# Performance work log

Measured on AMD Instinct MI355X. Metric: run time of the kernel, lower is better.

## Reference

```python
import jax, jax.numpy as jnp
import numpy as np

B = 1024      # number of states
NP = 32       # SVGD particles per state
AD = 20       # act_dim
OD = 64       # obs_dim
H = 256       # critic hidden width
STEPS = 5     # num_svgd_steps
LR = 0.1      # svgd_lr (adaptive_lr disabled)
SP0 = 1.0     # svgd_sigma_p0
ALIM = 1.0    # act_limit


def _q(obs, X, w1, b1, w2, b2, w3, b3):
    h = jnp.concatenate([obs, X], axis=-1)
    h = jax.nn.relu(h @ w1 + b1)
    h = jax.nn.relu(h @ w2 + b2)
    return jnp.squeeze(h @ w3 + b3, -1)


def _rbf(X):
    # X: [B, NP, AD] -> K [B,NP,NP], diff [B,NP,NP,AD], gamma [B,1,1], K_grad [B,NP,NP,AD]
    diff = X[:, :, None, :] - X[:, None, :, :]
    dist_sq = jnp.sum(diff * diff, axis=-1)
    # adaptive bandwidth via median heuristic (adaptive_sig=True)
    med = jnp.median(dist_sq.reshape(dist_sq.shape[0], -1), axis=-1)
    sig_sq = med / (2.0 * jnp.log(NP + 1.0))
    gamma = (1.0 / (2.0 * sig_sq + 1e-8))[:, None, None]
    K = jnp.exp(-gamma * dist_sq)
    K_grad = -2.0 * gamma[..., None] * diff * K[..., None]  # d/dx_i K(x_i, x_j)
    return K, diff, gamma, K_grad


def setup_inputs():
    key = jax.random.key(0)
    ks = jax.random.split(key, 16)
    N = B * NP

    def lin(k, fi, fo):
        return (jax.random.normal(k, (fi, fo), jnp.float32) / np.sqrt(fi)).astype(jnp.float32)

    return {
        "obs": jax.random.normal(ks[0], (N, OD), jnp.float32),
        "a0": jax.random.normal(ks[1], (N, AD), jnp.float32) * np.sqrt(SP0),
        "q1_w1": lin(ks[2], OD + AD, H), "q1_b1": jnp.zeros((H,), jnp.float32),
        "q1_w2": lin(ks[3], H, H),       "q1_b2": jnp.zeros((H,), jnp.float32),
        "q1_w3": lin(ks[4], H, 1),       "q1_b3": jnp.zeros((1,), jnp.float32),
        "q2_w1": lin(ks[5], OD + AD, H), "q2_b1": jnp.zeros((H,), jnp.float32),
        "q2_w2": lin(ks[6], H, H),       "q2_b2": jnp.zeros((H,), jnp.float32),
        "q2_w3": lin(ks[7], H, 1),       "q2_b3": jnp.zeros((1,), jnp.float32),
    }


def reference(obs, a0, q1_w1, q1_b1, q1_w2, q1_b2, q1_w3, q1_b3,
              q2_w1, q2_b1, q2_w2, q2_b2, q2_w3, q2_b3):
    eye = jnp.eye(NP, dtype=a0.dtype)

    def q_min_sum(Xf):
        q1 = _q(obs, Xf, q1_w1, q1_b1, q1_w2, q1_b2, q1_w3, q1_b3)
        q2 = _q(obs, Xf, q2_w1, q2_b1, q2_w2, q2_b2, q2_w3, q2_b3)
        return jnp.sum(jnp.minimum(q1, q2))

    score_fn = jax.grad(q_min_sum)  # autograd score function

    def step(carry, _):
        a, logp = carry
        score = score_fn(a).reshape(-1, NP, AD)                 # [B,NP,AD]
        X = a.reshape(-1, NP, AD)
        K, diff, gamma, Kg = _rbf(X)
        phi = (jnp.einsum('bij,bjd->bid', K, score) + Kg.sum(axis=1)) / NP
        # log-prob correction terms (with_logprob=True)
        term1 = jnp.mean(jnp.sum(Kg * score[:, None, :, :], axis=-1), axis=2)     # [B,NP]
        inner = jnp.sum(jnp.transpose(Kg, (0, 2, 1, 3)) * diff, axis=-1) \
                - AD * (K - eye)
        term2 = -2.0 * gamma[:, :, 0] * jnp.mean(inner, axis=1)                   # [B,NP]
        logp = logp - LR * (term1 + term2)
        a = a + LR * phi.reshape(a.shape)                        # svgd_optim
        return (a, logp), None

    logp0 = jnp.zeros((B, NP), a0.dtype)
    (a, logp_svgd), _ = jax.lax.scan(step, (a0, logp0), None, length=STEPS)

    a_sq = ALIM * jnp.tanh(a)                                    # [B*NP, AD]
    logp_normal = (-AD * 0.5 * jnp.log(2.0 * jnp.pi * SP0)
                   - 0.5 / SP0 * jnp.sum(a0 * a0, axis=-1)).reshape(-1, NP)
    logp_tanh = -jnp.sum(2.0 * (jnp.log(2.0) - a - jax.nn.softplus(-2.0 * a)),
                         axis=-1).reshape(-1, NP)
    logp_a = jnp.mean(logp_normal + logp_svgd + logp_tanh, axis=-1)  # [B]
    return a_sq, logp_a
```

## Files before the change

kernel.cpp:

```cpp
#include <hip/hip_runtime.h>
#include <math.h>

#define NPART 32
#define ADIM  20
#define ODIM  64
#define HID   256
#define NSTEPS 5
#define LRC   0.1f
#define NBLK  512
#define LOG33 3.4965075614664802f
#define A0LD  104

typedef short bf8 __attribute__((ext_vector_type(8)));
typedef short s4b __attribute__((ext_vector_type(4)));
typedef float f4  __attribute__((ext_vector_type(4)));
typedef unsigned u4 __attribute__((ext_vector_type(4)));

#define OW1T(n) ((n)*24576)
#define OW2T(n) (49152 + (n)*65536)
#define OW2C(n) (180224 + (n)*65536)
#define OW1X(n) (311296 + (n)*8192)
#define WS_ELEMS 327680

__device__ __forceinline__ short f2bf(float x) {
    unsigned u = __float_as_uint(x);
    u += 0x7FFFu + ((u >> 16) & 1u);
    return (short)(u >> 16);
}
__device__ __forceinline__ short f2bfT(float x) {
    return (short)(__float_as_uint(x) >> 16);
}
__device__ __forceinline__ float bf2f(short s) {
    return __uint_as_float(((unsigned)(unsigned short)s) << 16);
}

#define MFMA(a,b,c) __builtin_amdgcn_mfma_f32_16x16x32_bf16((a),(b),(c),0,0,0)

__global__ void prep_weights(const float* __restrict__ w1a, const float* __restrict__ w2a,
                             const float* __restrict__ w3a, const float* __restrict__ w1b,
                             const float* __restrict__ w2b, const float* __restrict__ w3b,
                             unsigned short* __restrict__ ws)
{
    int idx = blockIdx.x * 256 + threadIdx.x;
    if (idx >= WS_ELEMS) return;
    float val;
    if (idx < 49152) {
        int net = idx / 24576, rem = idx % 24576;
        int n = rem / 96, k = rem % 96;
        const float* w1 = net ? w1b : w1a;
        val = (k < 84) ? w1[k*256 + n] : 0.f;
    } else if (idx < 180224) {
        int t2 = idx - 49152; int net = t2 / 65536, rem = t2 % 65536;
        int n = rem / 256, k = rem % 256;
        const float* w2 = net ? w2b : w2a;
        val = w2[k*256 + n];
    } else if (idx < 311296) {
        int t2 = idx - 180224; int net = t2 / 65536, rem = t2 % 65536;
        const float* w2 = net ? w2b : w2a;
        const float* w3 = net ? w3b : w3a;
        val = w2[rem] * w3[rem % 256];
    } else {
        int t2 = idx - 311296; int net = t2 / 8192, rem = t2 % 8192;
        int d = rem / 256, n = rem % 256;
        const float* w1 = net ? w1b : w1a;
        val = (d < 20) ? w1[(64 + d)*256 + n] : 0.f;
    }
    ws[idx] = (unsigned short)f2bf(val);
}

__global__ void __launch_bounds__(512, 4)
svgd_main(const float* __restrict__ obs,  const float* __restrict__ a0g,
          const float* __restrict__ b1a,  const float* __restrict__ b2a, const float* __restrict__ b3a,
          const float* __restrict__ b1b,  const float* __restrict__ b2b, const float* __restrict__ b3b,
          const float* __restrict__ w3af, const float* __restrict__ w3bf,
          const unsigned short* __restrict__ ws, float* __restrict__ out)
{
    __shared__ __align__(16) short A0s[64*A0LD];
    __shared__ __align__(16) short hbuf[64*264];
    __shared__ unsigned maskS[2][2][64][8];
    __shared__ float Xm[64*20];
    __shared__ float scoreS[64*21];
    __shared__ float qpart[2][8][64];
    __shared__ int   winsS[64];
    __shared__ float logps[64];
    __shared__ unsigned short lutI[496], lutJ[496];
    __shared__ float med2[4];
    __shared__ float qvS[64];
    __shared__ float normsS[64], rowKS[64];
    __shared__ __align__(16) float diagS[64];

    float* d2sF = (float*)hbuf;
    float* GSF  = ((float*)hbuf) + 2304;
    short* SBs  = hbuf + 9216;
    short* KbS  = hbuf + 9216;
    short* STbS = hbuf + 11776;
    short* XTbS = hbuf + 14336;

    const int t = threadIdx.x, b = blockIdx.x;
    const int lane = t & 63, wv = t >> 6;
    const int q = lane >> 4, mp = lane & 15;
    const int nb = wv * 32;

    for (int p = t; p < 64*ODIM; p += 512) {
        int i = p >> 6, d = p & 63;
        A0s[i*A0LD + d] = f2bfT(obs[(b*64 + i)*ODIM + d]);
    }
    for (int p = t; p < 64*ADIM; p += 512) {
        int i = p / 20, d = p - i*20;
        float v = a0g[(b*64 + i)*20 + d];
        Xm[p] = v;
        A0s[i*A0LD + 64 + d] = f2bfT(v);
    }
    for (int p = t; p < 64*12; p += 512) { int i = p/12, d = p - i*12; A0s[i*A0LD + 84 + d] = 0; }
    if (t < 496) {
        int i_ = 0, rem = t;
        while (rem >= 31 - i_) { rem -= 31 - i_; ++i_; }
        lutI[t] = (unsigned short)i_; lutJ[t] = (unsigned short)(i_ + 1 + rem);
    }
    if (t < 64) logps[t] = 0.f;
    __syncthreads();

    for (int step = 0; step < NSTEPS; ++step) {
        for (int net = 0; net < 2; ++net) {
            const unsigned short* w1t = ws + OW1T(net);
            const unsigned short* w2t = ws + OW2T(net);
            const float* b1p = net ? b1b : b1a;
            const float* b2p = net ? b2b : b2a;
            const float* w3p = net ? w3bf : w3af;

            f4 acc[4][2];
            #pragma unroll
            for (int h = 0; h < 4; ++h) { acc[h][0] = (f4){0,0,0,0}; acc[h][1] = (f4){0,0,0,0}; }
            {
                const unsigned short* bp0 = w1t + (size_t)(nb +      mp)*96 + q*8;
                const unsigned short* bp1 = w1t + (size_t)(nb + 16 + mp)*96 + q*8;
                bf8 bb0 = *(const bf8*)bp0, bb1 = *(const bf8*)bp1;
                #pragma unroll
                for (int k0 = 0; k0 < 96; k0 += 32) {
                    bf8 n0 = bb0, n1 = bb1;
                    if (k0 + 32 < 96) { n0 = *(const bf8*)(bp0 + k0 + 32); n1 = *(const bf8*)(bp1 + k0 + 32); }
                    #pragma unroll
                    for (int h = 0; h < 4; ++h) {
                        bf8 aa = *(const bf8*)&A0s[(h*16 + mp)*A0LD + k0 + q*8];
                        acc[h][0] = MFMA(aa, bb0, acc[h][0]);
                        acc[h][1] = MFMA(aa, bb1, acc[h][1]);
                    }
                    bb0 = n0; bb1 = n1;
                }
            }
            {
                float bias0 = b1p[nb + mp], bias1 = b1p[nb + 16 + mp];
                #pragma unroll
                for (int h = 0; h < 4; ++h) {
                    #pragma unroll
                    for (int r = 0; r < 4; ++r) {
                        float v0 = acc[h][0][r] + bias0;
                        float v1 = acc[h][1][r] + bias1;
                        bool p0 = v0 > 0.f, p1 = v1 > 0.f;
                        unsigned long long bal0 = __ballot(p0);
                        unsigned long long bal1 = __ballot(p1);
                        int row = h*16 + q*4 + r;
                        hbuf[row*264 + nb +      mp] = f2bfT(p0 ? v0 : 0.f);
                        hbuf[row*264 + nb + 16 + mp] = f2bfT(p1 ? v1 : 0.f);
                        if (mp == 0) {
                            unsigned w = (unsigned)((bal0 >> (q*16)) & 0xFFFFull)
                                       | (((unsigned)((bal1 >> (q*16)) & 0xFFFFull)) << 16);
                            maskS[net][0][row][wv] = w;
                        }
                    }
                }
            }
            __syncthreads();

            #pragma unroll
            for (int h = 0; h < 4; ++h) { acc[h][0] = (f4){0,0,0,0}; acc[h][1] = (f4){0,0,0,0}; }
            {
                const unsigned short* bp0 = w2t + (size_t)(nb +      mp)*256 + q*8;
                const unsigned short* bp1 = w2t + (size_t)(nb + 16 + mp)*256 + q*8;
                bf8 bb0 = *(const bf8*)bp0, bb1 = *(const bf8*)bp1;
                #pragma unroll
                for (int k0 = 0; k0 < 256; k0 += 32) {
                    bf8 n0 = bb0, n1 = bb1;
                    if (k0 + 32 < 256) { n0 = *(const bf8*)(bp0 + k0 + 32); n1 = *(const bf8*)(bp1 + k0 + 32); }
                    #pragma unroll
                    for (int h = 0; h < 4; ++h) {
                        bf8 aa = *(const bf8*)&hbuf[(h*16 + mp)*264 + k0 + q*8];
                        acc[h][0] = MFMA(aa, bb0, acc[h][0]);
                        acc[h][1] = MFMA(aa, bb1, acc[h][1]);
                    }
                    bb0 = n0; bb1 = n1;
                }
            }
            {
                float bias0 = b2p[nb + mp], bias1 = b2p[nb + 16 + mp];
                float w30   = w3p[nb + mp], w31   = w3p[nb + 16 + mp];
                float qp[4][4] = {{0,0,0,0},{0,0,0,0},{0,0,0,0},{0,0,0,0}};
                #pragma unroll
                for (int h = 0; h < 4; ++h) {
                    #pragma unroll
                    for (int r = 0; r < 4; ++r) {
                        float v0 = acc[h][0][r] + bias0;
                        float v1 = acc[h][1][r] + bias1;
                        bool p0 = v0 > 0.f, p1 = v1 > 0.f;
                        unsigned long long bal0 = __ballot(p0);
                        unsigned long long bal1 = __ballot(p1);
                        if (mp == 0) {
                            unsigned w = (unsigned)((bal0 >> (q*16)) & 0xFFFFull)
                                       | (((unsigned)((bal1 >> (q*16)) & 0xFFFFull)) << 16);
                            maskS[net][1][h*16 + q*4 + r][wv] = w;
                        }
                        qp[h][r] += (p0 ? v0 * w30 : 0.f) + (p1 ? v1 * w31 : 0.f);
                    }
                }
                #pragma unroll
                for (int d = 1; d < 16; d <<= 1)
                    #pragma unroll
                    for (int h = 0; h < 4; ++h)
                        #pragma unroll
                        for (int r = 0; r < 4; ++r)
                            qp[h][r] += __shfl_xor(qp[h][r], d, 64);
                if (mp == 0) {
                    #pragma unroll
                    for (int h = 0; h < 4; ++h)
                        #pragma unroll
                        for (int r = 0; r < 4; ++r)
                            qpart[net][wv][h*16 + q*4 + r] = qp[h][r];
                }
            }
            __syncthreads();
        }

        if (t < 64) {
            float q0 = b3a[0], q1 = b3b[0];
            #pragma unroll
            for (int w = 0; w < 8; ++w) { q0 += qpart[0][w][t]; q1 += qpart[1][w][t]; }
            winsS[t] = (q0 <= q1) ? 0 : 1;
        }
        __syncthreads();

        for (int net = 0; net < 2; ++net) {
            const unsigned short* w2c = ws + OW2C(net);

            f4 acc[4][2];
            #pragma unroll
            for (int h = 0; h < 4; ++h) { acc[h][0] = (f4){0,0,0,0}; acc[h][1] = (f4){0,0,0,0}; }
            int win[4];
            #pragma unroll
            for (int h = 0; h < 4; ++h) win[h] = (winsS[h*16 + mp] == net);
            {
                const unsigned short* bp0 = w2c + (size_t)(nb +      mp)*256 + q*8;
                const unsigned short* bp1 = w2c + (size_t)(nb + 16 + mp)*256 + q*8;
                bf8 bb0 = *(const bf8*)bp0, bb1 = *(const bf8*)bp1;
                #pragma unroll
                for (int k0 = 0; k0 < 256; k0 += 32) {
                    bf8 n0 = bb0, n1 = bb1;
                    if (k0 + 32 < 256) { n0 = *(const bf8*)(bp0 + k0 + 32); n1 = *(const bf8*)(bp1 + k0 + 32); }
                    #pragma unroll
                    for (int h = 0; h < 4; ++h) {
                        unsigned bits = win[h] ? ((maskS[net][1][h*16 + mp][k0 >> 5] >> (q*8)) & 0xFFu) : 0u;
                        u4 mw;
                        mw[0] = ((bits &   1u) ? 0x3F80u : 0u) | ((bits &   2u) ? 0x3F800000u : 0u);
                        mw[1] = ((bits &   4u) ? 0x3F80u : 0u) | ((bits &   8u) ? 0x3F800000u : 0u);
                        mw[2] = ((bits &  16u) ? 0x3F80u : 0u) | ((bits &  32u) ? 0x3F800000u : 0u);
                        mw[3] = ((bits &  64u) ? 0x3F80u : 0u) | ((bits & 128u) ? 0x3F800000u : 0u);
                        bf8 aa = __builtin_bit_cast(bf8, mw);
                        acc[h][0] = MFMA(aa, bb0, acc[h][0]);
                        acc[h][1] = MFMA(aa, bb1, acc[h][1]);
                    }
                    bb0 = n0; bb1 = n1;
                }
            }
            #pragma unroll
            for (int h = 0; h < 4; ++h) {
                #pragma unroll
                for (int s = 0; s < 2; ++s) {
                    int col = nb + s*16 + mp;
                    #pragma unroll
                    for (int r = 0; r < 4; ++r) {
                        int row = h*16 + q*4 + r;
                        bool on = (maskS[net][0][row][col >> 5] >> (col & 31)) & 1u;
                        hbuf[row*264 + col] = f2bfT(on ? acc[h][s][r] : 0.f);
                    }
                }
            }
            __syncthreads();
            {
                int mt = wv & 3, ch = wv >> 2;
                const unsigned short* w1x = ws + OW1X(net);
                const unsigned short* bp  = w1x + (size_t)(ch*16 + mp)*256 + q*8;
                f4 sa = (f4){0,0,0,0};
                bf8 bx = *(const bf8*)bp;
                #pragma unroll
                for (int k0 = 0; k0 < 256; k0 += 32) {
                    bf8 nx = bx;
                    if (k0 + 32 < 256) nx = *(const bf8*)(bp + k0 + 32);
                    bf8 aa = *(const bf8*)&hbuf[(mt*16 + mp)*264 + k0 + q*8];
                    sa = MFMA(aa, bx, sa);
                    bx = nx;
                }
                int colD = ch*16 + mp;
                if (colD < 20) {
                    #pragma unroll
                    for (int r = 0; r < 4; ++r) {
                        int row = mt*16 + q*4 + r;
                        if (net == 0) scoreS[row*21 + colD]  = sa[r];
                        else          scoreS[row*21 + colD] += sa[r];
                    }
                }
            }
            __syncthreads();
        }

        if (t < 64) {
            int st = t >> 5;
            float nrm = 0.f, dg = 0.f;
            #pragma unroll
            for (int d = 0; d < 20; ++d) {
                float xb = bf2f(A0s[t*A0LD + 64 + d]);
                nrm += xb * xb;
                float sv = scoreS[t*21 + d];
                float xv = Xm[t*20 + d];
                dg += xv * sv;
                short sb = f2bfT(sv);
                SBs[t*40 + d] = sb;
                STbS[st*1280 + d*40 + (t & 31)] = sb;
                XTbS[st*1280 + d*40 + (t & 31)] = f2bfT(xv);
            }
            #pragma unroll
            for (int d = 20; d < 32; ++d) SBs[t*40 + d] = 0;
            normsS[t] = nrm;
            diagS[t]  = dg;
        }
        __syncthreads();

        {
            int stw = wv >> 2, mt = (wv >> 1) & 1, nt = wv & 1;
            bf8 aa  = *(const bf8*)&A0s[(stw*32 + mt*16 + mp)*A0LD + 64 + q*8];
            bf8 bbx = *(const bf8*)&A0s[(stw*32 + nt*16 + mp)*A0LD + 64 + q*8];
            bf8 bbs = *(const bf8*)&SBs[(stw*32 + nt*16 + mp)*40 + q*8];
            f4 gx = MFMA(aa, bbx, ((f4){0,0,0,0}));
            f4 gs = MFMA(aa, bbs, ((f4){0,0,0,0}));
            int jl = nt*16 + mp;
            float nj = normsS[stw*32 + jl];
            #pragma unroll
            for (int r = 0; r < 4; ++r) {
                int il = mt*16 + q*4 + r;
                d2sF[stw*1152 + il*36 + jl] = normsS[stw*32 + il] + nj - 2.f*gx[r];
                GSF [stw*1152 + il*36 + jl] = gs[r];
            }
        }
        __syncthreads();

        if (wv < 2) {
            const float* base = d2sF + wv*1152;
            float v[8];
            #pragma unroll
            for (int i = 0; i < 8; ++i) {
                int e = lane*8 + i;
                v[i] = (e < 496) ? base[lutI[e]*36 + lutJ[e]] : 3.4e38f;
            }
            for (int k = 2; k <= 512; k <<= 1) {
                for (int jj = k >> 1; jj >= 8; jj >>= 1) {
                    int lm = jj >> 3;
                    #pragma unroll
                    for (int i = 0; i < 8; ++i) {
                        float w = __shfl_xor(v[i], lm, 64);
                        int p = lane*8 + i;
                        bool takeMin = (((p & k) == 0) == ((p & jj) == 0));
                        v[i] = takeMin ? fminf(v[i], w) : fmaxf(v[i], w);
                    }
                }
                int jj0 = (k >> 1) < 4 ? (k >> 1) : 4;
                for (int jj = jj0; jj >= 1; jj >>= 1) {
                    #pragma unroll
                    for (int i = 0; i < 8; ++i) {
                        if ((i & jj) == 0) {
                            int i2 = i | jj;
                            int p = lane*8 + i;
                            bool up = ((p & k) == 0);
                            float x = v[i], y = v[i2];
                            float mn = fminf(x, y), mx = fmaxf(x, y);
                            v[i] = up ? mn : mx; v[i2] = up ? mx : mn;
                        }
                    }
                }
            }
            if (lane == 29) med2[wv*2 + 0] = v[7];
            if (lane == 30) med2[wv*2 + 1] = v[0];
        }
        __syncthreads();

        {
            int i = t >> 3, stw = i >> 5, il = i & 31, j0 = (t & 7) * 4;
            float medv = 0.5f * (med2[stw*2] + med2[stw*2 + 1]);
            float gam  = 1.f / (2.f * (medv / (2.f * LOG33)) + 1e-8f);
            f4 d2 = *(const f4*)&d2sF[stw*1152 + il*36 + j0];
            f4 gs = *(const f4*)&GSF [stw*1152 + il*36 + j0];
            f4 dg = *(const f4*)&diagS[stw*32 + j0];
            float K0 = expf(-gam * d2[0]), K1 = expf(-gam * d2[1]);
            float K2 = expf(-gam * d2[2]), K3 = expf(-gam * d2[3]);
            s4b kb; kb[0] = f2bfT(K0); kb[1] = f2bfT(K1); kb[2] = f2bfT(K2); kb[3] = f2bfT(K3);
            *(s4b*)&KbS[stw*1280 + il*40 + j0] = kb;
            float sK   = K0 + K1 + K2 + K3;
            float sKGS = K0*gs[0] + K1*gs[1] + K2*gs[2] + K3*gs[3];
            float sKd2 = K0*d2[0] + K1*d2[1] + K2*d2[2] + K3*d2[3];
            float sKdg = K0*dg[0] + K1*dg[1] + K2*dg[2] + K3*dg[3];
            #pragma unroll
            for (int d = 1; d < 8; d <<= 1) {
                sK   += __shfl_xor(sK,   d, 64);
                sKGS += __shfl_xor(sKGS, d, 64);
                sKd2 += __shfl_xor(sKd2, d, 64);
                sKdg += __shfl_xor(sKdg, d, 64);
            }
            if ((t & 7) == 0) {
                rowKS[i] = sK;
                float sdots = sKGS - sKdg;
                float ssum  = -2.f*gam*sdots
                              - 2.f*gam*(2.f*gam*sKd2 - 20.f*(sK - 1.f));
                logps[i] -= LRC * (ssum * (1.f/32.f));
            }
        }
        __syncthreads();

        {
            int stw = wv >> 2, mt = (wv >> 1) & 1, nt = wv & 1;
            float medv = 0.5f * (med2[stw*2] + med2[stw*2 + 1]);
            float gam  = 1.f / (2.f * (medv / (2.f * LOG33)) + 1e-8f);
            bf8 aa  = *(const bf8*)&KbS [stw*1280 + (mt*16 + mp)*40 + q*8];
            bf8 b1v = *(const bf8*)&STbS[stw*1280 + (nt*16 + mp)*40 + q*8];
            bf8 b2v = *(const bf8*)&XTbS[stw*1280 + (nt*16 + mp)*40 + q*8];
            f4 ks = MFMA(aa, b1v, ((f4){0,0,0,0}));
            f4 kx = MFMA(aa, b2v, ((f4){0,0,0,0}));
            int dd = nt*16 + mp;
            if (dd < 20) {
                #pragma unroll
                for (int r = 0; r < 4; ++r) {
                    int gi = stw*32 + mt*16 + q*4 + r;
                    float xi  = Xm[gi*20 + dd];
                    float phi = (ks[r] + 2.f*gam*(xi*rowKS[gi] - kx[r])) * (1.f/32.f);
                    float nx  = xi + LRC * phi;
                    Xm[gi*20 + dd] = nx;
                    A0s[gi*A0LD + 64 + dd] = f2bfT(nx);
                }
            }
        }
        __syncthreads();
    }

    for (int p = t; p < 64*20; p += 512) {
        int i = p / 20, d = p - i*20;
        out[(b*64 + i)*20 + d] = tanhf(Xm[p]);
    }
    if (t < 64) {
        float lt = 0.f, s0 = 0.f;
        for (int d = 0; d < 20; ++d) {
            float a  = Xm[t*20 + d];
            float x  = -2.f * a;
            float sp = fmaxf(x, 0.f) + log1pf(expf(-fabsf(x)));
            lt -= 2.f * (0.69314718056f - a - sp);
            float v = a0g[(b*64 + t)*20 + d];
            s0 += v * v;
        }
        qvS[t] = -18.3787706641f - 0.5f*s0 + logps[t] + lt;
    }
    __syncthreads();
    if (t < 2) {
        float s = 0.f;
        for (int i = 0; i < 32; ++i) s += qvS[t*32 + i];
        out[1024*32*20 + b*2 + t] = s * (1.f/32.f);
    }
}

extern "C" void kernel_launch(void* const* d_in, const int* in_sizes, int n_in,
                              void* d_out, int out_size, void* d_ws, size_t ws_size,
                              hipStream_t stream) {
    unsigned short* ws = (unsigned short*)d_ws;
    prep_weights<<<(WS_ELEMS + 255)/256, 256, 0, stream>>>(
        (const float*)d_in[2],  (const float*)d_in[4],  (const float*)d_in[6],
        (const float*)d_in[8],  (const float*)d_in[10], (const float*)d_in[12], ws);
    svgd_main<<<NBLK, 512, 0, stream>>>(
        (const float*)d_in[0],  (const float*)d_in[1],
        (const float*)d_in[3],  (const float*)d_in[5],  (const float*)d_in[7],
        (const float*)d_in[9],  (const float*)d_in[11], (const float*)d_in[13],
        (const float*)d_in[6],  (const float*)d_in[12],
        ws, (float*)d_out);
}
```

Measured before the change: 488.5 us.

## Process one state per block with 256 threads and wider per-wave N tiles

```diff
diff --git a/kernel.cpp b/kernel.cpp
--- a/kernel.cpp
+++ b/kernel.cpp
@@ -1,13 +1,9 @@
 #include <hip/hip_runtime.h>
 #include <math.h>
 
-#define NPART 32
-#define ADIM  20
-#define ODIM  64
-#define HID   256
 #define NSTEPS 5
 #define LRC   0.1f
-#define NBLK  512
+#define NBLK  1024
 #define LOG33 3.4965075614664802f
 #define A0LD  104
 
@@ -68,56 +64,55 @@
     ws[idx] = (unsigned short)f2bf(val);
 }
 
-__global__ void __launch_bounds__(512, 4)
+__global__ void __launch_bounds__(256, 4)
 svgd_main(const float* __restrict__ obs,  const float* __restrict__ a0g,
           const float* __restrict__ b1a,  const float* __restrict__ b2a, const float* __restrict__ b3a,
           const float* __restrict__ b1b,  const float* __restrict__ b2b, const float* __restrict__ b3b,
           const float* __restrict__ w3af, const float* __restrict__ w3bf,
           const unsigned short* __restrict__ ws, float* __restrict__ out)
 {
-    __shared__ __align__(16) short A0s[64*A0LD];
-    __shared__ __align__(16) short hbuf[64*264];
-    __shared__ unsigned maskS[2][2][64][8];
-    __shared__ float Xm[64*20];
-    __shared__ float scoreS[64*21];
-    __shared__ float qpart[2][8][64];
-    __shared__ int   winsS[64];
-    __shared__ float logps[64];
+    __shared__ __align__(16) short A0s[32*A0LD];
+    __shared__ __align__(16) short hbuf[32*264];
+    __shared__ unsigned maskS[2][2][32][9];
+    __shared__ float Xm[32*20];
+    __shared__ float scoreS[32*21];
+    __shared__ float qpart[2][4][32];
+    __shared__ float logps[32];
     __shared__ unsigned short lutI[496], lutJ[496];
-    __shared__ float med2[4];
-    __shared__ float qvS[64];
-    __shared__ float normsS[64], rowKS[64];
-    __shared__ __align__(16) float diagS[64];
+    __shared__ float med2[2];
+    __shared__ float qvS[32];
+    __shared__ float normsS[32], rowKS[32];
+    __shared__ __align__(16) float diagS[32];
 
     float* d2sF = (float*)hbuf;
-    float* GSF  = ((float*)hbuf) + 2304;
-    short* SBs  = hbuf + 9216;
-    short* KbS  = hbuf + 9216;
-    short* STbS = hbuf + 11776;
-    short* XTbS = hbuf + 14336;
+    float* GSF  = ((float*)hbuf) + 1152;
+    short* SBs  = hbuf + 4608;
+    short* KbS  = hbuf + 4608;
+    short* STbS = hbuf + 5888;
+    short* XTbS = hbuf + 7168;
 
     const int t = threadIdx.x, b = blockIdx.x;
     const int lane = t & 63, wv = t >> 6;
     const int q = lane >> 4, mp = lane & 15;
-    const int nb = wv * 32;
-
-    for (int p = t; p < 64*ODIM; p += 512) {
+    const int nb = wv * 64;
+
+    for (int p = t; p < 32*64; p += 256) {
         int i = p >> 6, d = p & 63;
-        A0s[i*A0LD + d] = f2bfT(obs[(b*64 + i)*ODIM + d]);
-    }
-    for (int p = t; p < 64*ADIM; p += 512) {
+        A0s[i*A0LD + d] = f2bfT(obs[(b*32 + i)*64 + d]);
+    }
+    for (int p = t; p < 32*20; p += 256) {
         int i = p / 20, d = p - i*20;
-        float v = a0g[(b*64 + i)*20 + d];
+        float v = a0g[(b*32 + i)*20 + d];
         Xm[p] = v;
         A0s[i*A0LD + 64 + d] = f2bfT(v);
     }
-    for (int p = t; p < 64*12; p += 512) { int i = p/12, d = p - i*12; A0s[i*A0LD + 84 + d] = 0; }
-    if (t < 496) {
-        int i_ = 0, rem = t;
+    for (int p = t; p < 32*12; p += 256) { int i = p/12, d = p - i*12; A0s[i*A0LD + 84 + d] = 0; }
+    for (int p = t; p < 496; p += 256) {
+        int i_ = 0, rem = p;
         while (rem >= 31 - i_) { rem -= 31 - i_; ++i_; }
-        lutI[t] = (unsigned short)i_; lutJ[t] = (unsigned short)(i_ + 1 + rem);
-    }
-    if (t < 64) logps[t] = 0.f;
+        lutI[p] = (unsigned short)i_; lutJ[p] = (unsigned short)(i_ + 1 + rem);
+    }
+    if (t < 32) logps[t] = 0.f;
     __syncthreads();
 
     for (int step = 0; step < NSTEPS; ++step) {
@@ -128,100 +123,110 @@
             const float* b2p = net ? b2b : b2a;
             const float* w3p = net ? w3bf : w3af;
 
-            f4 acc[4][2];
-            #pragma unroll
-            for (int h = 0; h < 4; ++h) { acc[h][0] = (f4){0,0,0,0}; acc[h][1] = (f4){0,0,0,0}; }
             {
-                const unsigned short* bp0 = w1t + (size_t)(nb +      mp)*96 + q*8;
-                const unsigned short* bp1 = w1t + (size_t)(nb + 16 + mp)*96 + q*8;
-                bf8 bb0 = *(const bf8*)bp0, bb1 = *(const bf8*)bp1;
+                f4 acc[2][4];
+                #pragma unroll
+                for (int h = 0; h < 2; ++h)
+                    #pragma unroll
+                    for (int s = 0; s < 4; ++s) acc[h][s] = (f4){0,0,0,0};
                 #pragma unroll
                 for (int k0 = 0; k0 < 96; k0 += 32) {
-                    bf8 n0 = bb0, n1 = bb1;
-                    if (k0 + 32 < 96) { n0 = *(const bf8*)(bp0 + k0 + 32); n1 = *(const bf8*)(bp1 + k0 + 32); }
-                    #pragma unroll
-                    for (int h = 0; h < 4; ++h) {
+                    bf8 bb[4];
+                    #pragma unroll
+                    for (int s = 0; s < 4; ++s)
+                        bb[s] = *(const bf8*)(w1t + (size_t)(nb + s*16 + mp)*96 + k0 + q*8);
+                    #pragma unroll
+                    for (int h = 0; h < 2; ++h) {
                         bf8 aa = *(const bf8*)&A0s[(h*16 + mp)*A0LD + k0 + q*8];
-                        acc[h][0] = MFMA(aa, bb0, acc[h][0]);
-                        acc[h][1] = MFMA(aa, bb1, acc[h][1]);
-                    }
-                    bb0 = n0; bb1 = n1;
-                }
-            }
+                        #pragma unroll
+                        for (int s = 0; s < 4; ++s) acc[h][s] = MFMA(aa, bb[s], acc[h][s]);
+                    }
+                }
+                float bias[4];
+                #pragma unroll
+                for (int s = 0; s < 4; ++s) bias[s] = b1p[nb + s*16 + mp];
+                #pragma unroll
+                for (int h = 0; h < 2; ++h) {
+                    #pragma unroll
+                    for (int r = 0; r < 4; ++r) {
+                        unsigned long long bal[4];
+                        #pragma unroll
+                        for (int s = 0; s < 4; ++s) {
+                            float v = acc[h][s][r] + bias[s];
+                            bool pos = v > 0.f;
+                            bal[s] = __ballot(pos);
+                            hbuf[(h*16 + q*4 + r)*264 + nb + s*16 + mp] = f2bfT(pos ? v : 0.f);
+                        }
+                        if (mp == 0) {
+                            int row = h*16 + q*4 + r;
+                            unsigned w01 = (unsigned)((bal[0] >> (q*16)) & 0xFFFFull)
+                                         | (((unsigned)((bal[1] >> (q*16)) & 0xFFFFull)) << 16);
+                            unsigned w23 = (unsigned)((bal[2] >> (q*16)) & 0xFFFFull)
+                                         | (((unsigned)((bal[3] >> (q*16)) & 0xFFFFull)) << 16);
+                            maskS[net][0][row][wv*2 + 0] = w01;
+                            maskS[net][0][row][wv*2 + 1] = w23;
+                        }
+                    }
+                }
+            }
+            __syncthreads();
+
             {
-                float bias0 = b1p[nb + mp], bias1 = b1p[nb + 16 + mp];
-                #pragma unroll
-                for (int h = 0; h < 4; ++h) {
+                f4 acc[2][4];
+                #pragma unroll
+                for (int h = 0; h < 2; ++h)
+                    #pragma unroll
+                    for (int s = 0; s < 4; ++s) acc[h][s] = (f4){0,0,0,0};
+                #pragma unroll
+                for (int k0 = 0; k0 < 256; k0 += 32) {
+                    bf8 bb[4];
+                    #pragma unroll
+                    for (int s = 0; s < 4; ++s)
+                        bb[s] = *(const bf8*)(w2t + (size_t)(nb + s*16 + mp)*256 + k0 + q*8);
+                    #pragma unroll
+                    for (int h = 0; h < 2; ++h) {
+                        bf8 aa = *(const bf8*)&hbuf[(h*16 + mp)*264 + k0 + q*8];
+                        #pragma unroll
+                        for (int s = 0; s < 4; ++s) acc[h][s] = MFMA(aa, bb[s], acc[h][s]);
+                    }
+                }
+                float bias[4], w3v[4];
+                #pragma unroll
+                for (int s = 0; s < 4; ++s) { bias[s] = b2p[nb + s*16 + mp]; w3v[s] = w3p[nb + s*16 + mp]; }
+                float qp[2][4] = {{0,0,0,0},{0,0,0,0}};
+                #pragma unroll
+                for (int h = 0; h < 2; ++h) {
                     #pragma unroll
                     for (int r = 0; r < 4; ++r) {
-                        float v0 = acc[h][0][r] + bias0;
-                        float v1 = acc[h][1][r] + bias1;
-                        bool p0 = v0 > 0.f, p1 = v1 > 0.f;
-                        unsigned long long bal0 = __ballot(p0);
-                        unsigned long long bal1 = __ballot(p1);
-                        int row = h*16 + q*4 + r;
-                        hbuf[row*264 + nb +      mp] = f2bfT(p0 ? v0 : 0.f);
-                        hbuf[row*264 + nb + 16 + mp] = f2bfT(p1 ? v1 : 0.f);
+                        unsigned long long bal[4];
+                        #pragma unroll
+                        for (int s = 0; s < 4; ++s) {
+                            float v = acc[h][s][r] + bias[s];
+                            bool pos = v > 0.f;
+                            bal[s] = __ballot(pos);
+                            qp[h][r] += pos ? v * w3v[s] : 0.f;
+                        }
                         if (mp == 0) {
-                            unsigned w = (unsigned)((bal0 >> (q*16)) & 0xFFFFull)
-                                       | (((unsigned)((bal1 >> (q*16)) & 0xFFFFull)) << 16);
-                            maskS[net][0][row][wv] = w;
+                            int row = h*16 + q*4 + r;
+                            unsigned w01 = (unsigned)((bal[0] >> (q*16)) & 0xFFFFull)
+                                         | (((unsigned)((bal[1] >> (q*16)) & 0xFFFFull)) << 16);
+                            unsigned w23 = (unsigned)((bal[2] >> (q*16)) & 0xFFFFull)
+                                         | (((unsigned)((bal[3] >> (q*16)) & 0xFFFFull)) << 16);
+                            maskS[net][1][row][wv*2 + 0] = w01;
+                            maskS[net][1][row][wv*2 + 1] = w23;
                         }
                     }
                 }
-            }
-            __syncthreads();
-
-            #pragma unroll
-            for (int h = 0; h < 4; ++h) { acc[h][0] = (f4){0,0,0,0}; acc[h][1] = (f4){0,0,0,0}; }
-            {
-                const unsigned short* bp0 = w2t + (size_t)(nb +      mp)*256 + q*8;
-                const unsigned short* bp1 = w2t + (size_t)(nb + 16 + mp)*256 + q*8;
-                bf8 bb0 = *(const bf8*)bp0, bb1 = *(const bf8*)bp1;
-                #pragma unroll
-                for (int k0 = 0; k0 < 256; k0 += 32) {
-                    bf8 n0 = bb0, n1 = bb1;
-                    if (k0 + 32 < 256) { n0 = *(const bf8*)(bp0 + k0 + 32); n1 = *(const bf8*)(bp1 + k0 + 32); }
-                    #pragma unroll
-                    for (int h = 0; h < 4; ++h) {
-                        bf8 aa = *(const bf8*)&hbuf[(h*16 + mp)*264 + k0 + q*8];
-                        acc[h][0] = MFMA(aa, bb0, acc[h][0]);
-                        acc[h][1] = MFMA(aa, bb1, acc[h][1]);
-                    }
-                    bb0 = n0; bb1 = n1;
-                }
-            }
-            {
-                float bias0 = b2p[nb + mp], bias1 = b2p[nb + 16 + mp];
-                float w30   = w3p[nb + mp], w31   = w3p[nb + 16 + mp];
-                float qp[4][4] = {{0,0,0,0},{0,0,0,0},{0,0,0,0},{0,0,0,0}};
-                #pragma unroll
-                for (int h = 0; h < 4; ++h) {
-                    #pragma unroll
-                    for (int r = 0; r < 4; ++r) {
-                        float v0 = acc[h][0][r] + bias0;
-                        float v1 = acc[h][1][r] + bias1;
-                        bool p0 = v0 > 0.f, p1 = v1 > 0.f;
-                        unsigned long long bal0 = __ballot(p0);
-                        unsigned long long bal1 = __ballot(p1);
-                        if (mp == 0) {
-                            unsigned w = (unsigned)((bal0 >> (q*16)) & 0xFFFFull)
-                                       | (((unsigned)((bal1 >> (q*16)) & 0xFFFFull)) << 16);
-                            maskS[net][1][h*16 + q*4 + r][wv] = w;
-                        }
-                        qp[h][r] += (p0 ? v0 * w30 : 0.f) + (p1 ? v1 * w31 : 0.f);
-                    }
-                }
                 #pragma unroll
                 for (int d = 1; d < 16; d <<= 1)
                     #pragma unroll
-                    for (int h = 0; h < 4; ++h)
+                    for (int h = 0; h < 2; ++h)
                         #pragma unroll
                         for (int r = 0; r < 4; ++r)
                             qp[h][r] += __shfl_xor(qp[h][r], d, 64);
                 if (mp == 0) {
                     #pragma unroll
-                    for (int h = 0; h < 4; ++h)
+                    for (int h = 0; h < 2; ++h)
                         #pragma unroll
                         for (int r = 0; r < 4; ++r)
                             qpart[net][wv][h*16 + q*4 + r] = qp[h][r];
@@ -230,73 +235,71 @@
             __syncthreads();
         }
 
-        if (t < 64) {
-            float q0 = b3a[0], q1 = b3b[0];
+        int winf[2][2];
+        {
+            float ba = b3a[0], bb_ = b3b[0];
             #pragma unroll
-            for (int w = 0; w < 8; ++w) { q0 += qpart[0][w][t]; q1 += qpart[1][w][t]; }
-            winsS[t] = (q0 <= q1) ? 0 : 1;
-        }
-        __syncthreads();
-
+            for (int h = 0; h < 2; ++h) {
+                int row = h*16 + mp;
+                float q0 = ba, q1 = bb_;
+                #pragma unroll
+                for (int w = 0; w < 4; ++w) { q0 += qpart[0][w][row]; q1 += qpart[1][w][row]; }
+                winf[0][h] = (q0 <= q1) ? 1 : 0;
+                winf[1][h] = 1 - winf[0][h];
+            }
+        }
+        #pragma unroll
         for (int net = 0; net < 2; ++net) {
             const unsigned short* w2c = ws + OW2C(net);
-
-            f4 acc[4][2];
-            #pragma unroll
-            for (int h = 0; h < 4; ++h) { acc[h][0] = (f4){0,0,0,0}; acc[h][1] = (f4){0,0,0,0}; }
-            int win[4];
-            #pragma unroll
-            for (int h = 0; h < 4; ++h) win[h] = (winsS[h*16 + mp] == net);
             {
-                const unsigned short* bp0 = w2c + (size_t)(nb +      mp)*256 + q*8;
-                const unsigned short* bp1 = w2c + (size_t)(nb + 16 + mp)*256 + q*8;
-                bf8 bb0 = *(const bf8*)bp0, bb1 = *(const bf8*)bp1;
+                f4 acc[2][4];
+                #pragma unroll
+                for (int h = 0; h < 2; ++h)
+                    #pragma unroll
+                    for (int s = 0; s < 4; ++s) acc[h][s] = (f4){0,0,0,0};
                 #pragma unroll
                 for (int k0 = 0; k0 < 256; k0 += 32) {
-                    bf8 n0 = bb0, n1 = bb1;
-                    if (k0 + 32 < 256) { n0 = *(const bf8*)(bp0 + k0 + 32); n1 = *(const bf8*)(bp1 + k0 + 32); }
-                    #pragma unroll
-                    for (int h = 0; h < 4; ++h) {
-                        unsigned bits = win[h] ? ((maskS[net][1][h*16 + mp][k0 >> 5] >> (q*8)) & 0xFFu) : 0u;
+                    bf8 bb[4];
+                    #pragma unroll
+                    for (int s = 0; s < 4; ++s)
+                        bb[s] = *(const bf8*)(w2c + (size_t)(nb + s*16 + mp)*256 + k0 + q*8);
+                    #pragma unroll
+                    for (int h = 0; h < 2; ++h) {
+                        unsigned bits = winf[net][h] ? ((maskS[net][1][h*16 + mp][k0 >> 5] >> (q*8)) & 0xFFu) : 0u;
                         u4 mw;
                         mw[0] = ((bits &   1u) ? 0x3F80u : 0u) | ((bits &   2u) ? 0x3F800000u : 0u);
                         mw[1] = ((bits &   4u) ? 0x3F80u : 0u) | ((bits &   8u) ? 0x3F800000u : 0u);
                         mw[2] = ((bits &  16u) ? 0x3F80u : 0u) | ((bits &  32u) ? 0x3F800000u : 0u);
                         mw[3] = ((bits &  64u) ? 0x3F80u : 0u) | ((bits & 128u) ? 0x3F800000u : 0u);
                         bf8 aa = __builtin_bit_cast(bf8, mw);
-                        acc[h][0] = MFMA(aa, bb0, acc[h][0]);
-                        acc[h][1] = MFMA(aa, bb1, acc[h][1]);
-                    }
-                    bb0 = n0; bb1 = n1;
-                }
-            }
-            #pragma unroll
-            for (int h = 0; h < 4; ++h) {
-                #pragma unroll
-                for (int s = 0; s < 2; ++s) {
-                    int col = nb + s*16 + mp;
-                    #pragma unroll
-                    for (int r = 0; r < 4; ++r) {
-                        int row = h*16 + q*4 + r;
-                        bool on = (maskS[net][0][row][col >> 5] >> (col & 31)) & 1u;
-                        hbuf[row*264 + col] = f2bfT(on ? acc[h][s][r] : 0.f);
+                        #pragma unroll
+                        for (int s = 0; s < 4; ++s) acc[h][s] = MFMA(aa, bb[s], acc[h][s]);
+                    }
+                }
+                #pragma unroll
+                for (int h = 0; h < 2; ++h) {
+                    #pragma unroll
+                    for (int s = 0; s < 4; ++s) {
+                        int col = nb + s*16 + mp;
+                        #pragma unroll
+                        for (int r = 0; r < 4; ++r) {
+                            int row = h*16 + q*4 + r;
+                            bool on = (maskS[net][0][row][col >> 5] >> (col & 31)) & 1u;
+                            hbuf[row*264 + col] = f2bfT(on ? acc[h][s][r] : 0.f);
+                        }
                     }
                 }
             }
             __syncthreads();
             {
-                int mt = wv & 3, ch = wv >> 2;
-                const unsigned short* w1x = ws + OW1X(net);
-                const unsigned short* bp  = w1x + (size_t)(ch*16 + mp)*256 + q*8;
+                int mt = wv & 1, ch = wv >> 1;
+                const unsigned short* bp = ws + OW1X(net) + (size_t)(ch*16 + mp)*256 + q*8;
                 f4 sa = (f4){0,0,0,0};
-                bf8 bx = *(const bf8*)bp;
                 #pragma unroll
                 for (int k0 = 0; k0 < 256; k0 += 32) {
-                    bf8 nx = bx;
-                    if (k0 + 32 < 256) nx = *(const bf8*)(bp + k0 + 32);
+                    bf8 bx = *(const bf8*)(bp + k0);
                     bf8 aa = *(const bf8*)&hbuf[(mt*16 + mp)*264 + k0 + q*8];
                     sa = MFMA(aa, bx, sa);
-                    bx = nx;
                 }
                 int colD = ch*16 + mp;
                 if (colD < 20) {
@@ -311,53 +314,59 @@
             __syncthreads();
         }
 
-        if (t < 64) {
-            int st = t >> 5;
+        {
+            int i = t >> 3, j = t & 7;
             float nrm = 0.f, dg = 0.f;
             #pragma unroll
-            for (int d = 0; d < 20; ++d) {
-                float xb = bf2f(A0s[t*A0LD + 64 + d]);
-                nrm += xb * xb;
-                float sv = scoreS[t*21 + d];
-                float xv = Xm[t*20 + d];
-                dg += xv * sv;
-                short sb = f2bfT(sv);
-                SBs[t*40 + d] = sb;
-                STbS[st*1280 + d*40 + (t & 31)] = sb;
-                XTbS[st*1280 + d*40 + (t & 31)] = f2bfT(xv);
-            }
+            for (int dd = 0; dd < 3; ++dd) {
+                int d = j + dd*8;
+                if (d < 20) {
+                    float xb = bf2f(A0s[i*A0LD + 64 + d]);
+                    nrm += xb * xb;
+                    float sv = scoreS[i*21 + d];
+                    float xv = Xm[i*20 + d];
+                    dg += xv * sv;
+                    short sb = f2bfT(sv);
+                    SBs[i*40 + d] = sb;
+                    STbS[d*40 + i] = sb;
+                    XTbS[d*40 + i] = f2bfT(xv);
+                }
+            }
+            SBs[i*40 + 20 + j] = 0;
+            if (j < 4) SBs[i*40 + 28 + j] = 0;
             #pragma unroll
-            for (int d = 20; d < 32; ++d) SBs[t*40 + d] = 0;
-            normsS[t] = nrm;
-            diagS[t]  = dg;
+            for (int d = 1; d < 8; d <<= 1) {
+                nrm += __shfl_xor(nrm, d, 64);
+                dg  += __shfl_xor(dg,  d, 64);
+            }
+            if (j == 0) { normsS[i] = nrm; diagS[i] = dg; }
         }
         __syncthreads();
 
         {
-            int stw = wv >> 2, mt = (wv >> 1) & 1, nt = wv & 1;
-            bf8 aa  = *(const bf8*)&A0s[(stw*32 + mt*16 + mp)*A0LD + 64 + q*8];
-            bf8 bbx = *(const bf8*)&A0s[(stw*32 + nt*16 + mp)*A0LD + 64 + q*8];
-            bf8 bbs = *(const bf8*)&SBs[(stw*32 + nt*16 + mp)*40 + q*8];
+            int mt = (wv >> 1) & 1, nt = wv & 1;
+            bf8 aa  = *(const bf8*)&A0s[(mt*16 + mp)*A0LD + 64 + q*8];
+            bf8 bbx = *(const bf8*)&A0s[(nt*16 + mp)*A0LD + 64 + q*8];
+            bf8 bbs = *(const bf8*)&SBs[(nt*16 + mp)*40 + q*8];
             f4 gx = MFMA(aa, bbx, ((f4){0,0,0,0}));
             f4 gs = MFMA(aa, bbs, ((f4){0,0,0,0}));
             int jl = nt*16 + mp;
-            float nj = normsS[stw*32 + jl];
+            float nj = normsS[jl];
             #pragma unroll
             for (int r = 0; r < 4; ++r) {
                 int il = mt*16 + q*4 + r;
-                d2sF[stw*1152 + il*36 + jl] = normsS[stw*32 + il] + nj - 2.f*gx[r];
-                GSF [stw*1152 + il*36 + jl] = gs[r];
+                d2sF[il*36 + jl] = normsS[il] + nj - 2.f*gx[r];
+                GSF [il*36 + jl] = gs[r];
             }
         }
         __syncthreads();
 
-        if (wv < 2) {
-            const float* base = d2sF + wv*1152;
+        if (wv == 0) {
             float v[8];
             #pragma unroll
             for (int i = 0; i < 8; ++i) {
                 int e = lane*8 + i;
-                v[i] = (e < 496) ? base[lutI[e]*36 + lutJ[e]] : 3.4e38f;
+                v[i] = (e < 496) ? d2sF[lutI[e]*36 + lutJ[e]] : 3.4e38f;
             }
             for (int k = 2; k <= 512; k <<= 1) {
                 for (int jj = k >> 1; jj >= 8; jj >>= 1) {
@@ -385,22 +394,22 @@
                     }
                 }
             }
-            if (lane == 29) med2[wv*2 + 0] = v[7];
-            if (lane == 30) med2[wv*2 + 1] = v[0];
+            if (lane == 29) med2[0] = v[7];
+            if (lane == 30) med2[1] = v[0];
         }
         __syncthreads();
 
         {
-            int i = t >> 3, stw = i >> 5, il = i & 31, j0 = (t & 7) * 4;
-            float medv = 0.5f * (med2[stw*2] + med2[stw*2 + 1]);
+            int il = t >> 3, j0 = (t & 7) * 4;
+            float medv = 0.5f * (med2[0] + med2[1]);
             float gam  = 1.f / (2.f * (medv / (2.f * LOG33)) + 1e-8f);
-            f4 d2 = *(const f4*)&d2sF[stw*1152 + il*36 + j0];
-            f4 gs = *(const f4*)&GSF [stw*1152 + il*36 + j0];
-            f4 dg = *(const f4*)&diagS[stw*32 + j0];
-            float K0 = expf(-gam * d2[0]), K1 = expf(-gam * d2[1]);
-            float K2 = expf(-gam * d2[2]), K3 = expf(-gam * d2[3]);
+            f4 d2 = *(const f4*)&d2sF[il*36 + j0];
+            f4 gs = *(const f4*)&GSF [il*36 + j0];
+            f4 dg = *(const f4*)&diagS[j0];
+            float K0 = __expf(-gam * d2[0]), K1 = __expf(-gam * d2[1]);
+            float K2 = __expf(-gam * d2[2]), K3 = __expf(-gam * d2[3]);
             s4b kb; kb[0] = f2bfT(K0); kb[1] = f2bfT(K1); kb[2] = f2bfT(K2); kb[3] = f2bfT(K3);
-            *(s4b*)&KbS[stw*1280 + il*40 + j0] = kb;
+            *(s4b*)&KbS[il*40 + j0] = kb;
             float sK   = K0 + K1 + K2 + K3;
             float sKGS = K0*gs[0] + K1*gs[1] + K2*gs[2] + K3*gs[3];
             float sKd2 = K0*d2[0] + K1*d2[1] + K2*d2[2] + K3*d2[3];
@@ -413,29 +422,29 @@
                 sKdg += __shfl_xor(sKdg, d, 64);
             }
             if ((t & 7) == 0) {
-                rowKS[i] = sK;
+                rowKS[il] = sK;
                 float sdots = sKGS - sKdg;
                 float ssum  = -2.f*gam*sdots
                               - 2.f*gam*(2.f*gam*sKd2 - 20.f*(sK - 1.f));
-                logps[i] -= LRC * (ssum * (1.f/32.f));
+                logps[il] -= LRC * (ssum * (1.f/32.f));
             }
         }
         __syncthreads();
 
         {
-            int stw = wv >> 2, mt = (wv >> 1) & 1, nt = wv & 1;
-            float medv = 0.5f * (med2[stw*2] + med2[stw*2 + 1]);
+            int mt = (wv >> 1) & 1, nt = wv & 1;
+            float medv = 0.5f * (med2[0] + med2[1]);
             float gam  = 1.f / (2.f * (medv / (2.f * LOG33)) + 1e-8f);
-            bf8 aa  = *(const bf8*)&KbS [stw*1280 + (mt*16 + mp)*40 + q*8];
-            bf8 b1v = *(const bf8*)&STbS[stw*1280 + (nt*16 + mp)*40 + q*8];
-            bf8 b2v = *(const bf8*)&XTbS[stw*1280 + (nt*16 + mp)*40 + q*8];
+            bf8 aa  = *(const bf8*)&KbS [(mt*16 + mp)*40 + q*8];
+            bf8 b1v = *(const bf8*)&STbS[(nt*16 + mp)*40 + q*8];
+            bf8 b2v = *(const bf8*)&XTbS[(nt*16 + mp)*40 + q*8];
             f4 ks = MFMA(aa, b1v, ((f4){0,0,0,0}));
             f4 kx = MFMA(aa, b2v, ((f4){0,0,0,0}));
             int dd = nt*16 + mp;
             if (dd < 20) {
                 #pragma unroll
                 for (int r = 0; r < 4; ++r) {
-                    int gi = stw*32 + mt*16 + q*4 + r;
+                    int gi = mt*16 + q*4 + r;
                     float xi  = Xm[gi*20 + dd];
                     float phi = (ks[r] + 2.f*gam*(xi*rowKS[gi] - kx[r])) * (1.f/32.f);
                     float nx  = xi + LRC * phi;
@@ -447,27 +456,38 @@
         __syncthreads();
     }
 
-    for (int p = t; p < 64*20; p += 512) {
+    for (int p = t; p < 32*20; p += 256) {
         int i = p / 20, d = p - i*20;
-        out[(b*64 + i)*20 + d] = tanhf(Xm[p]);
-    }
-    if (t < 64) {
+        out[(b*32 + i)*20 + d] = tanhf(Xm[p]);
+    }
+    {
+        int i = t >> 3, j = t & 7;
         float lt = 0.f, s0 = 0.f;
-        for (int d = 0; d < 20; ++d) {
-            float a  = Xm[t*20 + d];
-            float x  = -2.f * a;
-            float sp = fmaxf(x, 0.f) + log1pf(expf(-fabsf(x)));
-            lt -= 2.f * (0.69314718056f - a - sp);
-            float v = a0g[(b*64 + t)*20 + d];
-            s0 += v * v;
-        }
-        qvS[t] = -18.3787706641f - 0.5f*s0 + logps[t] + lt;
+        #pragma unroll
+        for (int dd = 0; dd < 3; ++dd) {
+            int d = j + dd*8;
+            if (d < 20) {
+                float a  = Xm[i*20 + d];
+                float x  = -2.f * a;
+                float sp = fmaxf(x, 0.f) + log1pf(__expf(-fabsf(x)));
+                lt -= 2.f * (0.69314718056f - a - sp);
+                float v = a0g[(b*32 + i)*20 + d];
+                s0 += v * v;
+            }
+        }
+        #pragma unroll
+        for (int d = 1; d < 8; d <<= 1) {
+            lt += __shfl_xor(lt, d, 64);
+            s0 += __shfl_xor(s0, d, 64);
+        }
+        if (j == 0) qvS[i] = -18.3787706641f - 0.5f*s0 + logps[i] + lt;
     }
     __syncthreads();
-    if (t < 2) {
-        float s = 0.f;
-        for (int i = 0; i < 32; ++i) s += qvS[t*32 + i];
-        out[1024*32*20 + b*2 + t] = s * (1.f/32.f);
+    if (t < 32) {
+        float v = qvS[t];
+        #pragma unroll
+        for (int d = 1; d < 32; d <<= 1) v += __shfl_xor(v, d, 32);
+        if (t == 0) out[1024*32*20 + b] = v * (1.f/32.f);
     }
 }
 
@@ -478,7 +498,7 @@
     prep_weights<<<(WS_ELEMS + 255)/256, 256, 0, stream>>>(
         (const float*)d_in[2],  (const float*)d_in[4],  (const float*)d_in[6],
         (const float*)d_in[8],  (const float*)d_in[10], (const float*)d_in[12], ws);
-    svgd_main<<<NBLK, 512, 0, stream>>>(
+    svgd_main<<<NBLK, 256, 0, stream>>>(
         (const float*)d_in[0],  (const float*)d_in[1],
         (const float*)d_in[3],  (const float*)d_in[5],  (const float*)d_in[7],
         (const float*)d_in[9],  (const float*)d_in[11], (const float*)d_in[13],
```

After: 957.4 us. 1.96x slower.
